# Kernel tuning notes

Hardware: AMD Instinct MI355X
Metric: run time of the kernel (lower is better)

## Reference

```python
import jax, jax.numpy as jnp
import numpy as np

BINS = 256
SIGMA = 3.0
DELTA = 1.0 / BINS
CENTERS = DELTA * (jnp.arange(BINS, dtype=jnp.float32) + 0.5)  # min=0
W1 = W2 = W3 = 1.0

# --- soft histogram (SoftHistTorch with bins=256, min=0, max=1, sigma=3) ---

def _soft_hist(flat):
    # flat: [N] -> hist: [BINS]
    d = flat[None, :] - CENTERS[:, None]                      # [BINS, N]
    h = jax.nn.sigmoid(SIGMA * (d + DELTA / 2)) - jax.nn.sigmoid(SIGMA * (d - DELTA / 2))
    return h.sum(axis=1)


def _color_uniform(x):
    # x: [B,H,W]; uniform_loss = mean_b sum_bins h*log(h) (only where h>0)
    flat = x.reshape(x.shape[0], -1)
    hist = jax.vmap(_soft_hist)(flat)                          # [B, BINS]
    safe = jnp.where(hist > 0, hist, 1.0)
    hlogh = jnp.where(hist > 0, hist * jnp.log(safe), 0.0)
    return hlogh.sum(axis=1).mean()

# --- SSIM (standard pytorch-ssim: 11x11 gaussian window, sigma=1.5, 1 channel) ---

def _gauss_window(size=11, sigma=1.5):
    c = np.arange(size, dtype=np.float64) - size // 2
    g = np.exp(-(c ** 2) / (2.0 * sigma ** 2))
    g /= g.sum()
    w = np.outer(g, g)
    return jnp.asarray(w, dtype=jnp.float32)[None, None]       # [1,1,11,11]

_WIN = _gauss_window()
_PAD = 11 // 2


def _conv(img):
    return jax.lax.conv_general_dilated(img, _WIN, (1, 1), [(_PAD, _PAD), (_PAD, _PAD)])


def _ssim(img1, img2):
    C1, C2 = 0.01 ** 2, 0.03 ** 2
    mu1, mu2 = _conv(img1), _conv(img2)
    mu1_sq, mu2_sq, mu1_mu2 = mu1 * mu1, mu2 * mu2, mu1 * mu2
    s1 = _conv(img1 * img1) - mu1_sq
    s2 = _conv(img2 * img2) - mu2_sq
    s12 = _conv(img1 * img2) - mu1_mu2
    num = (2 * mu1_mu2 + C1) * (2 * s12 + C2)
    den = (mu1_sq + mu2_sq + C1) * (s1 + s2 + C2)
    return (num / den).mean()


def _norm01(t):
    t = t - t.min()
    return t / t.max()


def setup_inputs() -> dict:
    key = jax.random.key(0)
    k1, k2, k3 = jax.random.split(key, 3)
    x = jax.random.uniform(k1, (8, 1, 384, 384), dtype=jnp.float32)
    target = jax.random.uniform(k2, (8, 384, 384), dtype=jnp.float32)
    depth = jax.random.uniform(k3, (8, 384, 384), dtype=jnp.float32)
    return {"x": x, "target": target, "depth": depth}


def reference(x, target, depth):
    x = jnp.squeeze(x, 1)                 # [B,H,W]
    output = _norm01(x)                   # torch in-place normalization aliases x
    IR = _norm01(target)
    depth_n = _norm01(depth)
    B = x.shape[0]
    uniform_loss = _color_uniform(output)
    depth_loss = jnp.sum(output * depth_n) / B   # x aliases normalized output in torch
    ssim_loss = 1.0 - _ssim(output[:, None], IR[:, None])
    loss = W1 * 1e-06 * uniform_loss + W2 * 1e-05 * depth_loss + W3 * ssim_loss
    return loss
```

## Files before the change

### kernel.cpp

```cpp
#include <hip/hip_runtime.h>
#include <math.h>

#define NTHR 256
#define K_FINE 2048
#define HW 147456
#define N1 1179648
#define IMG 384
#define NHC 16
#define NCHUNK 128
#define NTILE 1152
#define TOTAL (NTILE + NCHUNK)
#define NSOFT 256

#define WS_PMM  0
#define WS_SUM  1536
#define WS_CTR  2304
#define WS_HIST 2312
#define WS_SSIM (WS_HIST + 8*K_FINE)
#define WS_UNIF (WS_SSIM + NTILE)

#define HRS (42*33)
#define SMEMF (42*43*2 + 3*HRS)

__global__ __launch_bounds__(NTHR) void k_minmax(
        const float* __restrict__ x, const float* __restrict__ tg,
        const float* __restrict__ dp, float* __restrict__ wsf)
{
    __shared__ float swred[4][12];
    const int tid = threadIdx.x, bid = blockIdx.x;
    const float4* x4 = (const float4*)x  + bid * 1152;
    const float4* t4 = (const float4*)tg + bid * 1152;
    const float4* d4 = (const float4*)dp + bid * 1152;
    float mn0 = 3.4e38f, mx0 = -3.4e38f;
    float mn1 = 3.4e38f, mx1 = -3.4e38f;
    float mn2 = 3.4e38f, mx2 = -3.4e38f;
    float sx = 0.f, sd = 0.f, sxd = 0.f;
    for (int i = tid; i < 1152; i += NTHR) {
        float4 a = x4[i], b = t4[i], d = d4[i];
        mn0 = fminf(mn0, fminf(fminf(a.x, a.y), fminf(a.z, a.w)));
        mx0 = fmaxf(mx0, fmaxf(fmaxf(a.x, a.y), fmaxf(a.z, a.w)));
        mn1 = fminf(mn1, fminf(fminf(b.x, b.y), fminf(b.z, b.w)));
        mx1 = fmaxf(mx1, fmaxf(fmaxf(b.x, b.y), fmaxf(b.z, b.w)));
        mn2 = fminf(mn2, fminf(fminf(d.x, d.y), fminf(d.z, d.w)));
        mx2 = fmaxf(mx2, fmaxf(fmaxf(d.x, d.y), fmaxf(d.z, d.w)));
        sx += (a.x + a.y) + (a.z + a.w);
        sd += (d.x + d.y) + (d.z + d.w);
        sxd = fmaf(a.x, d.x, fmaf(a.y, d.y, fmaf(a.z, d.z, fmaf(a.w, d.w, sxd))));
    }
    #pragma unroll
    for (int off = 32; off; off >>= 1) {
        mn0 = fminf(mn0, __shfl_down(mn0, off, 64));
        mx0 = fmaxf(mx0, __shfl_down(mx0, off, 64));
        mn1 = fminf(mn1, __shfl_down(mn1, off, 64));
        mx1 = fmaxf(mx1, __shfl_down(mx1, off, 64));
        mn2 = fminf(mn2, __shfl_down(mn2, off, 64));
        mx2 = fmaxf(mx2, __shfl_down(mx2, off, 64));
        sx  += __shfl_down(sx,  off, 64);
        sd  += __shfl_down(sd,  off, 64);
        sxd += __shfl_down(sxd, off, 64);
    }
    if ((tid & 63) == 0) {
        int w = tid >> 6;
        swred[w][0] = mn0; swred[w][1] = mx0; swred[w][2] = mn1;
        swred[w][3] = mx1; swred[w][4] = mn2; swred[w][5] = mx2;
        swred[w][6] = sxd; swred[w][7] = sx;  swred[w][8] = sd;
    }
    __syncthreads();
    if (tid == 0) {
        #pragma unroll
        for (int w = 1; w < 4; w++) {
            swred[0][0] = fminf(swred[0][0], swred[w][0]);
            swred[0][1] = fmaxf(swred[0][1], swred[w][1]);
            swred[0][2] = fminf(swred[0][2], swred[w][2]);
            swred[0][3] = fmaxf(swred[0][3], swred[w][3]);
            swred[0][4] = fminf(swred[0][4], swred[w][4]);
            swred[0][5] = fmaxf(swred[0][5], swred[w][5]);
            swred[0][6] += swred[w][6];
            swred[0][7] += swred[w][7];
            swred[0][8] += swred[w][8];
        }
        wsf[WS_PMM +        bid * 2]     = swred[0][0];
        wsf[WS_PMM +        bid * 2 + 1] = swred[0][1];
        wsf[WS_PMM + 512  + bid * 2]     = swred[0][2];
        wsf[WS_PMM + 512  + bid * 2 + 1] = swred[0][3];
        wsf[WS_PMM + 1024 + bid * 2]     = swred[0][4];
        wsf[WS_PMM + 1024 + bid * 2 + 1] = swred[0][5];
        wsf[WS_SUM +        bid] = swred[0][6];
        wsf[WS_SUM + 256  + bid] = swred[0][7];
        wsf[WS_SUM + 512  + bid] = swred[0][8];
        if (bid == 0) ((int*)wsf)[WS_CTR] = 0;
    }
    if (tid < 64) ((int*)wsf)[WS_HIST + bid * 64 + tid] = 0;
}

__device__ __forceinline__ void reduce_minmax(
        const float* __restrict__ wsf, float swred[4][12], int tid,
        float& xmn, float& xinv, float& tmn, float& tinv, float& dmn, float& dinv)
{
    const float2* pm = (const float2*)&wsf[WS_PMM];
    float2 a = pm[tid], b = pm[256 + tid], c = pm[512 + tid];
    float mn0 = a.x, mx0 = a.y, mn1 = b.x, mx1 = b.y, mn2 = c.x, mx2 = c.y;
    #pragma unroll
    for (int off = 32; off; off >>= 1) {
        mn0 = fminf(mn0, __shfl_down(mn0, off, 64));
        mx0 = fmaxf(mx0, __shfl_down(mx0, off, 64));
        mn1 = fminf(mn1, __shfl_down(mn1, off, 64));
        mx1 = fmaxf(mx1, __shfl_down(mx1, off, 64));
        mn2 = fminf(mn2, __shfl_down(mn2, off, 64));
        mx2 = fmaxf(mx2, __shfl_down(mx2, off, 64));
    }
    if ((tid & 63) == 0) {
        int w = tid >> 6;
        swred[w][0] = mn0; swred[w][1] = mx0; swred[w][2] = mn1;
        swred[w][3] = mx1; swred[w][4] = mn2; swred[w][5] = mx2;
    }
    __syncthreads();
    mn0 = fminf(fminf(swred[0][0], swred[1][0]), fminf(swred[2][0], swred[3][0]));
    mx0 = fmaxf(fmaxf(swred[0][1], swred[1][1]), fmaxf(swred[2][1], swred[3][1]));
    mn1 = fminf(fminf(swred[0][2], swred[1][2]), fminf(swred[2][2], swred[3][2]));
    mx1 = fmaxf(fmaxf(swred[0][3], swred[1][3]), fmaxf(swred[2][3], swred[3][3]));
    mn2 = fminf(fminf(swred[0][4], swred[1][4]), fminf(swred[2][4], swred[3][4]));
    mx2 = fmaxf(fmaxf(swred[0][5], swred[1][5]), fmaxf(swred[2][5], swred[3][5]));
    xmn = mn0; xinv = 1.0f / (mx0 - mn0);
    tmn = mn1; tinv = 1.0f / (mx1 - mn1);
    dmn = mn2; dinv = 1.0f / (mx2 - mn2);
    __syncthreads();
}

__global__ __launch_bounds__(NTHR) void k_work(
        const float* __restrict__ x, const float* __restrict__ tg,
        float* __restrict__ wsf)
{
    __shared__ float smem[SMEMF];
    __shared__ float swred[4][12];
    const int tid = threadIdx.x, bid = blockIdx.x;

    float xmn, xinv, tmn, tinv, dmn, dinv;
    reduce_minmax(wsf, swred, tid, xmn, xinv, tmn, tinv, dmn, dinv);
    (void)dmn; (void)dinv;

    if (bid < NTILE) {
        float g[11];
        {
            float s = 0.f;
            #pragma unroll
            for (int i = 0; i < 11; i++) {
                float dd = (float)(i - 5);
                g[i] = expf(-dd * dd / 4.5f);
                s += g[i];
            }
            float is = 1.0f / s;
            #pragma unroll
            for (int i = 0; i < 11; i++) g[i] *= is;
        }
        float* sO  = smem;
        float* sI  = smem + 42 * 43;
        float* hr0 = smem + 2 * 42 * 43;
        float* hr1 = hr0 + HRS;
        float* hr2 = hr1 + HRS;
        int img = bid / 144;
        int tl  = bid % 144;
        int ty0 = (tl / 12) * 32 - 5;
        int tx0 = (tl % 12) * 32 - 5;
        const float* xb = x  + (size_t)img * HW;
        const float* tb = tg + (size_t)img * HW;
        for (int idx = tid; idx < 42 * 42; idx += NTHR) {
            int rr = idx / 42, cc = idx % 42;
            int gy = ty0 + rr, gx = tx0 + cc;
            float xv = 0.f, tv = 0.f;
            if (gy >= 0 && gy < IMG && gx >= 0 && gx < IMG) {
                int o = gy * IMG + gx;
                xv = (xb[o] - xmn) * xinv;
                tv = (tb[o] - tmn) * tinv;
            }
            sO[rr * 43 + cc] = xv; sI[rr * 43 + cc] = tv;
        }
        __syncthreads();
        for (int idx = tid; idx < 42 * 32; idx += NTHR) {
            int rr = idx >> 5, cx = idx & 31;
            const float* rowO = sO + rr * 43 + cx;
            const float* rowI = sI + rr * 43 + cx;
            float so = 0, si = 0;
            #pragma unroll
            for (int d = 0; d < 11; d++) { so += g[d] * rowO[d]; si += g[d] * rowI[d]; }
            hr0[rr * 33 + cx] = so; hr1[rr * 33 + cx] = si;
        }
        __syncthreads();
        const int ox = tid & 31, oy0 = (tid >> 5) << 2;
        float mu1[4], mu2[4];
        {
            float w0[14], w1[14];
            #pragma unroll
            for (int k = 0; k < 14; k++) {
                int hb = (oy0 + k) * 33 + ox;
                w0[k] = hr0[hb]; w1[k] = hr1[hb];
            }
            #pragma unroll
            for (int p = 0; p < 4; p++) {
                float m1 = 0, m2 = 0;
                #pragma unroll
                for (int dy = 0; dy < 11; dy++) {
                    m1 += g[dy] * w0[p + dy];
                    m2 += g[dy] * w1[p + dy];
                }
                mu1[p] = m1; mu2[p] = m2;
            }
        }
        __syncthreads();
        for (int idx = tid; idx < 42 * 32; idx += NTHR) {
            int rr = idx >> 5, cx = idx & 31;
            const float* rowO = sO + rr * 43 + cx;
            const float* rowI = sI + rr * 43 + cx;
            float soo = 0, sii = 0, soi = 0;
            #pragma unroll
            for (int d = 0; d < 11; d++) {
                float o = rowO[d], ii = rowI[d], w = g[d];
                soo += w * o * o; sii += w * ii * ii; soi += w * o * ii;
            }
            int hb = rr * 33 + cx;
            hr0[hb] = soo; hr1[hb] = sii; hr2[hb] = soi;
        }
        __syncthreads();
        const float C1 = 1e-4f, C2 = 9e-4f;
        float lsum = 0.f;
        {
            float w0[14], w1[14], w2[14];
            #pragma unroll
            for (int k = 0; k < 14; k++) {
                int hb = (oy0 + k) * 33 + ox;
                w0[k] = hr0[hb]; w1[k] = hr1[hb]; w2[k] = hr2[hb];
            }
            #pragma unroll
            for (int p = 0; p < 4; p++) {
                float m11 = 0, m22 = 0, m12 = 0;
                #pragma unroll
                for (int dy = 0; dy < 11; dy++) {
                    float w = g[dy];
                    m11 += w * w0[p + dy];
                    m22 += w * w1[p + dy];
                    m12 += w * w2[p + dy];
                }
                float mu1s = mu1[p] * mu1[p], mu2s = mu2[p] * mu2[p];
                float mu12 = mu1[p] * mu2[p];
                float s1 = m11 - mu1s, s2 = m22 - mu2s, s12 = m12 - mu12;
                lsum += ((2.f * mu12 + C1) * (2.f * s12 + C2))
                      / ((mu1s + mu2s + C1) * (s1 + s2 + C2));
            }
        }
        #pragma unroll
        for (int off = 32; off; off >>= 1) lsum += __shfl_down(lsum, off, 64);
        if ((tid & 63) == 0) swred[tid >> 6][6] = lsum;
        __syncthreads();
        if (tid == 0)
            wsf[WS_SSIM + bid] = swred[0][6] + swred[1][6] + swred[2][6] + swred[3][6];
    } else {
        int c = bid - NTILE;
        int* lh = (int*)smem;
        for (int i = tid; i < K_FINE; i += NTHR) lh[i] = 0;
        __syncthreads();
        int batch = c >> 4, chunk = c & 15;
        const float4* x4 = (const float4*)x + (size_t)batch * (HW / 4) + chunk * 2304;
        for (int i = tid; i < 2304; i += NTHR) {
            float4 xv = x4[i];
            float o0 = (xv.x - xmn) * xinv, o1 = (xv.y - xmn) * xinv;
            float o2 = (xv.z - xmn) * xinv, o3 = (xv.w - xmn) * xinv;
            int j0 = min(K_FINE - 1, max(0, (int)(o0 * K_FINE)));
            int j1 = min(K_FINE - 1, max(0, (int)(o1 * K_FINE)));
            int j2 = min(K_FINE - 1, max(0, (int)(o2 * K_FINE)));
            int j3 = min(K_FINE - 1, max(0, (int)(o3 * K_FINE)));
            atomicAdd(lh + j0, 1); atomicAdd(lh + j1, 1);
            atomicAdd(lh + j2, 1); atomicAdd(lh + j3, 1);
        }
        __syncthreads();
        int* gh = (int*)wsf + WS_HIST + batch * K_FINE;
        for (int i = tid; i < K_FINE; i += NTHR) {
            int v = lh[i];
            if (v) atomicAdd(gh + i, v);
        }
    }
}

__global__ __launch_bounds__(NTHR) void k_soft_final(
        float* __restrict__ wsf, float* __restrict__ out)
{
    __shared__ int lh[K_FINE];
    __shared__ float swred[4][12];
    __shared__ float s8[8];
    __shared__ int amLast;
    const int tid = threadIdx.x, bid = blockIdx.x;
    int batch = bid >> 5;
    const int* gh = (const int*)wsf + WS_HIST + batch * K_FINE;
    for (int i = tid; i < K_FINE; i += NTHR) lh[i] = gh[i];
    __syncthreads();
    int binLocal = tid >> 5, slice = tid & 31;
    int bin = (bid & 31) * 8 + binLocal;
    const float delta = 1.0f / 256.0f;
    const float r   = expf(3.0f * delta);
    const float rm1 = r - 1.0f;
    const float c32 = expf(-3.0f * 32.0f / (float)K_FINE);
    float L = (float)bin * delta;
    float u = expf(3.0f * (L - ((float)slice + 0.5f) * (1.0f / (float)K_FINE)));
    float h = 0.f;
    #pragma unroll 4
    for (int j = slice; j < K_FINE; j += 32) {
        float cnt = (float)lh[j];
        float t1 = 1.0f + u;
        float t2 = fmaf(u, r, 1.0f);
        h = fmaf(cnt * (u * rm1), __builtin_amdgcn_rcpf(t1 * t2), h);
        u *= c32;
    }
    #pragma unroll
    for (int off = 16; off; off >>= 1) h += __shfl_down(h, off, 32);
    if (slice == 0) s8[binLocal] = h;
    __syncthreads();
    if (tid == 0) {
        float hl = 0.f;
        #pragma unroll
        for (int b = 0; b < 8; b++) {
            float hh = s8[b];
            hl += (hh > 0.f) ? hh * logf(hh) : 0.f;
        }
        wsf[WS_UNIF + bid] = hl;
        __threadfence();
        int old = atomicAdd((int*)wsf + WS_CTR, 1);
        amLast = (old == NSOFT - 1);
    }
    __syncthreads();
    if (!amLast) return;

    __threadfence();
    float xmn, xinv, tmn, tinv, dmn, dinv;
    reduce_minmax(wsf, swred, tid, xmn, xinv, tmn, tinv, dmn, dinv);
    (void)tmn; (void)tinv;
    float sxd  = wsf[WS_SUM + tid];
    float sx   = wsf[WS_SUM + 256 + tid];
    float sd   = wsf[WS_SUM + 512 + tid];
    float bsum = 0.f;
    for (int i = tid; i < NTILE; i += NTHR) bsum += wsf[WS_SSIM + i];
    float c = wsf[WS_UNIF + tid];
    float* r0 = (float*)lh;
    float* r1 = r0 + 256; float* r2 = r1 + 256;
    float* r3 = r2 + 256; float* r4 = r3 + 256;
    r0[tid] = sxd; r1[tid] = sx; r2[tid] = sd; r3[tid] = bsum; r4[tid] = c;
    __syncthreads();
    for (int s = 128; s; s >>= 1) {
        if (tid < s) {
            r0[tid] += r0[tid + s]; r1[tid] += r1[tid + s];
            r2[tid] += r2[tid + s]; r3[tid] += r3[tid + s];
            r4[tid] += r4[tid + s];
        }
        __syncthreads();
    }
    if (tid == 0) {
        float SXD = r0[0], SX = r1[0], SD = r2[0];
        float uniform  = r4[0] / 8.0f;
        float depthNum = SXD - xmn * SD - dmn * SX + (float)N1 * xmn * dmn;
        float depthL   = xinv * dinv * depthNum / 8.0f;
        float ssimMean = r3[0] / (float)N1;
        out[0] = 1e-6f * uniform + 1e-5f * depthL + (1.0f - ssimMean);
    }
}

extern "C" void kernel_launch(void* const* d_in, const int* in_sizes, int n_in,
                              void* d_out, int out_size, void* d_ws, size_t ws_size,
                              hipStream_t stream) {
    const float* x  = (const float*)d_in[0];
    const float* tg = (const float*)d_in[1];
    const float* dp = (const float*)d_in[2];
    float* wsf = (float*)d_ws;
    float* out = (float*)d_out;
    hipLaunchKernelGGL(k_minmax,     dim3(256),   dim3(NTHR), 0, stream, x, tg, dp, wsf);
    hipLaunchKernelGGL(k_work,       dim3(TOTAL), dim3(NTHR), 0, stream, x, tg, wsf);
    hipLaunchKernelGGL(k_soft_final, dim3(NSOFT), dim3(NTHR), 0, stream, wsf, out);
}
```

Measured before the change: 39.74 us.

## Fuse SSIM horizontal pass with global loads and compute all five planes at once

The SSIM tile no longer stages normalized x/target tiles in shared memory. Each thread reads 11 pixels directly from global memory and computes all five horizontal convolution sums (mu and second moments) in one pass. The vertical pass then runs over five shared planes without the intermediate barriers. This removes two shared-memory passes and two syncs, at the cost of redundant global loads (each pixel is read about 11 times, mostly hitting cache) and higher register pressure.

```diff
diff --git a/kernel.cpp b/kernel.cpp
--- a/kernel.cpp
+++ b/kernel.cpp
@@ -20,7 +20,7 @@
 #define WS_UNIF (WS_SSIM + NTILE)
 
 #define HRS (42*33)
-#define SMEMF (42*43*2 + 3*HRS)
+#define SMEMF (5*HRS)
 
 __global__ __launch_bounds__(NTHR) void k_minmax(
         const float* __restrict__ x, const float* __restrict__ tg,
@@ -153,99 +153,87 @@
             #pragma unroll
             for (int i = 0; i < 11; i++) g[i] *= is;
         }
-        float* sO  = smem;
-        float* sI  = smem + 42 * 43;
-        float* hr0 = smem + 2 * 42 * 43;
+        float* hr0 = smem;
         float* hr1 = hr0 + HRS;
         float* hr2 = hr1 + HRS;
+        float* hr3 = hr2 + HRS;
+        float* hr4 = hr3 + HRS;
         int img = bid / 144;
         int tl  = bid % 144;
         int ty0 = (tl / 12) * 32 - 5;
         int tx0 = (tl % 12) * 32 - 5;
         const float* xb = x  + (size_t)img * HW;
         const float* tb = tg + (size_t)img * HW;
-        for (int idx = tid; idx < 42 * 42; idx += NTHR) {
-            int rr = idx / 42, cc = idx % 42;
-            int gy = ty0 + rr, gx = tx0 + cc;
-            float xv = 0.f, tv = 0.f;
-            if (gy >= 0 && gy < IMG && gx >= 0 && gx < IMG) {
-                int o = gy * IMG + gx;
-                xv = (xb[o] - xmn) * xinv;
-                tv = (tb[o] - tmn) * tinv;
+
+        for (int t = tid; t < 42 * 33; t += NTHR) {
+            int rr = t / 33, cx = t - rr * 33;
+            int gy = ty0 + rr, b = tx0 + cx;
+            float o[11], ii[11];
+            bool rowOK = ((unsigned)gy < (unsigned)IMG);
+            if (rowOK && b >= 0 && b + 10 < IMG) {
+                const float* po = xb + gy * IMG + b;
+                const float* pi = tb + gy * IMG + b;
+                #pragma unroll
+                for (int k = 0; k < 11; k++) {
+                    o[k]  = (po[k] - xmn) * xinv;
+                    ii[k] = (pi[k] - tmn) * tinv;
+                }
+            } else {
+                #pragma unroll
+                for (int k = 0; k < 11; k++) {
+                    int gx = b + k;
+                    bool okk = rowOK && ((unsigned)gx < (unsigned)IMG);
+                    float xv = 0.f, tv = 0.f;
+                    if (okk) {
+                        int off = gy * IMG + gx;
+                        xv = (xb[off] - xmn) * xinv;
+                        tv = (tb[off] - tmn) * tinv;
+                    }
+                    o[k] = xv; ii[k] = tv;
+                }
             }
-            sO[rr * 43 + cc] = xv; sI[rr * 43 + cc] = tv;
-        }
-        __syncthreads();
-        for (int idx = tid; idx < 42 * 32; idx += NTHR) {
-            int rr = idx >> 5, cx = idx & 31;
-            const float* rowO = sO + rr * 43 + cx;
-            const float* rowI = sI + rr * 43 + cx;
-            float so = 0, si = 0;
+            float c1 = 0, c2 = 0, c3 = 0, c4 = 0, c5 = 0;
             #pragma unroll
-            for (int d = 0; d < 11; d++) { so += g[d] * rowO[d]; si += g[d] * rowI[d]; }
-            hr0[rr * 33 + cx] = so; hr1[rr * 33 + cx] = si;
-        }
-        __syncthreads();
+            for (int k = 0; k < 11; k++) {
+                float gk = g[k];
+                float go = gk * o[k], gi = gk * ii[k];
+                c1 = fmaf(gk, o[k], c1);
+                c2 = fmaf(gk, ii[k], c2);
+                c3 = fmaf(go, o[k], c3);
+                c4 = fmaf(gi, ii[k], c4);
+                c5 = fmaf(go, ii[k], c5);
+            }
+            hr0[t] = c1; hr1[t] = c2; hr2[t] = c3; hr3[t] = c4; hr4[t] = c5;
+        }
+        __syncthreads();
+
         const int ox = tid & 31, oy0 = (tid >> 5) << 2;
-        float mu1[4], mu2[4];
-        {
-            float w0[14], w1[14];
-            #pragma unroll
-            for (int k = 0; k < 14; k++) {
-                int hb = (oy0 + k) * 33 + ox;
-                w0[k] = hr0[hb]; w1[k] = hr1[hb];
-            }
-            #pragma unroll
-            for (int p = 0; p < 4; p++) {
-                float m1 = 0, m2 = 0;
-                #pragma unroll
-                for (int dy = 0; dy < 11; dy++) {
-                    m1 += g[dy] * w0[p + dy];
-                    m2 += g[dy] * w1[p + dy];
-                }
-                mu1[p] = m1; mu2[p] = m2;
-            }
-        }
-        __syncthreads();
-        for (int idx = tid; idx < 42 * 32; idx += NTHR) {
-            int rr = idx >> 5, cx = idx & 31;
-            const float* rowO = sO + rr * 43 + cx;
-            const float* rowI = sI + rr * 43 + cx;
-            float soo = 0, sii = 0, soi = 0;
-            #pragma unroll
-            for (int d = 0; d < 11; d++) {
-                float o = rowO[d], ii = rowI[d], w = g[d];
-                soo += w * o * o; sii += w * ii * ii; soi += w * o * ii;
-            }
-            int hb = rr * 33 + cx;
-            hr0[hb] = soo; hr1[hb] = sii; hr2[hb] = soi;
-        }
-        __syncthreads();
+        float a1[4], a2[4], b11[4], b22[4], b12[4];
+        #define VCONV(HR, ACC)                                              \
+        {                                                                   \
+            float w[14];                                                    \
+            _Pragma("unroll")                                               \
+            for (int k = 0; k < 14; k++) w[k] = HR[(oy0 + k) * 33 + ox];    \
+            _Pragma("unroll")                                               \
+            for (int p = 0; p < 4; p++) {                                   \
+                float m = 0.f;                                              \
+                _Pragma("unroll")                                           \
+                for (int dy = 0; dy < 11; dy++) m = fmaf(g[dy], w[p + dy], m); \
+                ACC[p] = m;                                                 \
+            }                                                               \
+        }
+        VCONV(hr0, a1) VCONV(hr1, a2) VCONV(hr2, b11) VCONV(hr3, b22) VCONV(hr4, b12)
+        #undef VCONV
+
         const float C1 = 1e-4f, C2 = 9e-4f;
         float lsum = 0.f;
-        {
-            float w0[14], w1[14], w2[14];
-            #pragma unroll
-            for (int k = 0; k < 14; k++) {
-                int hb = (oy0 + k) * 33 + ox;
-                w0[k] = hr0[hb]; w1[k] = hr1[hb]; w2[k] = hr2[hb];
-            }
-            #pragma unroll
-            for (int p = 0; p < 4; p++) {
-                float m11 = 0, m22 = 0, m12 = 0;
-                #pragma unroll
-                for (int dy = 0; dy < 11; dy++) {
-                    float w = g[dy];
-                    m11 += w * w0[p + dy];
-                    m22 += w * w1[p + dy];
-                    m12 += w * w2[p + dy];
-                }
-                float mu1s = mu1[p] * mu1[p], mu2s = mu2[p] * mu2[p];
-                float mu12 = mu1[p] * mu2[p];
-                float s1 = m11 - mu1s, s2 = m22 - mu2s, s12 = m12 - mu12;
-                lsum += ((2.f * mu12 + C1) * (2.f * s12 + C2))
-                      / ((mu1s + mu2s + C1) * (s1 + s2 + C2));
-            }
+        #pragma unroll
+        for (int p = 0; p < 4; p++) {
+            float mu1s = a1[p] * a1[p], mu2s = a2[p] * a2[p];
+            float mu12 = a1[p] * a2[p];
+            float s1 = b11[p] - mu1s, s2 = b22[p] - mu2s, s12 = b12[p] - mu12;
+            lsum += ((2.f * mu12 + C1) * (2.f * s12 + C2))
+                  / ((mu1s + mu2s + C1) * (s1 + s2 + C2));
         }
         #pragma unroll
         for (int off = 32; off; off >>= 1) lsum += __shfl_down(lsum, off, 64);
```

Measured after the change: 51.85 us. 30.5% more time.

## Fuse soft-histogram and final reduction into work kernel via atomic tail blocks

Applied to the files above, without the earlier changes.

Removes the third kernel launch. The last 256 blocks to finish the work kernel, ordered by an atomic rank counter, wait until all histogram blocks are done and then compute the soft histogram. The very last of those blocks spins until every block has finished and writes the final loss. Histogram blocks are moved to the front of the grid so they finish early, and the SSIM convolutions use explicit fmaf. In exchange, the code relies on spin-waits and relaxed/acquire atomics for cross-block ordering, and the tail blocks run serially after the main work.

```diff
diff --git a/kernel.cpp b/kernel.cpp
--- a/kernel.cpp
+++ b/kernel.cpp
@@ -6,7 +6,6 @@
 #define HW 147456
 #define N1 1179648
 #define IMG 384
-#define NHC 16
 #define NCHUNK 128
 #define NTILE 1152
 #define TOTAL (NTILE + NCHUNK)
@@ -19,8 +18,23 @@
 #define WS_SSIM (WS_HIST + 8*K_FINE)
 #define WS_UNIF (WS_SSIM + NTILE)
 
+#define CTR_FIN  0
+#define CTR_HIST 1
+#define CTR_SOFT 2
+
 #define HRS (42*33)
 #define SMEMF (42*43*2 + 3*HRS)
+
+#define AGENT __HIP_MEMORY_SCOPE_AGENT
+
+__device__ __forceinline__ void spin_relaxed_then_acq(int* p, int target) {
+    while (__hip_atomic_load(p, __ATOMIC_RELAXED, AGENT) < target)
+        __builtin_amdgcn_s_sleep(16);
+    (void)__hip_atomic_load(p, __ATOMIC_ACQUIRE, AGENT);
+}
+__device__ __forceinline__ void drain_vmem() {
+    asm volatile("s_waitcnt vmcnt(0)" ::: "memory");
+}
 
 __global__ __launch_bounds__(NTHR) void k_minmax(
         const float* __restrict__ x, const float* __restrict__ tg,
@@ -88,9 +102,9 @@
         wsf[WS_SUM +        bid] = swred[0][6];
         wsf[WS_SUM + 256  + bid] = swred[0][7];
         wsf[WS_SUM + 512  + bid] = swred[0][8];
-        if (bid == 0) ((int*)wsf)[WS_CTR] = 0;
     }
     if (tid < 64) ((int*)wsf)[WS_HIST + bid * 64 + tid] = 0;
+    if (bid == 0 && tid < 8) ((int*)wsf)[WS_CTR + tid] = 0;
 }
 
 __device__ __forceinline__ void reduce_minmax(
@@ -129,17 +143,46 @@
 
 __global__ __launch_bounds__(NTHR) void k_work(
         const float* __restrict__ x, const float* __restrict__ tg,
-        float* __restrict__ wsf)
+        float* __restrict__ wsf, float* __restrict__ out)
 {
     __shared__ float smem[SMEMF];
     __shared__ float swred[4][12];
+    __shared__ float s8[8];
+    __shared__ int sbc[2];
     const int tid = threadIdx.x, bid = blockIdx.x;
+    int* ctr = (int*)wsf + WS_CTR;
 
     float xmn, xinv, tmn, tinv, dmn, dinv;
     reduce_minmax(wsf, swred, tid, xmn, xinv, tmn, tinv, dmn, dinv);
     (void)dmn; (void)dinv;
 
-    if (bid < NTILE) {
+    const bool isHist = (bid < NCHUNK);
+    if (isHist) {
+        int c = bid;
+        int* lh = (int*)smem;
+        for (int i = tid; i < K_FINE; i += NTHR) lh[i] = 0;
+        __syncthreads();
+        int batch = c >> 4, chunk = c & 15;
+        const float4* x4 = (const float4*)x + (size_t)batch * (HW / 4) + chunk * 2304;
+        for (int i = tid; i < 2304; i += NTHR) {
+            float4 xv = x4[i];
+            float o0 = (xv.x - xmn) * xinv, o1 = (xv.y - xmn) * xinv;
+            float o2 = (xv.z - xmn) * xinv, o3 = (xv.w - xmn) * xinv;
+            int j0 = min(K_FINE - 1, max(0, (int)(o0 * K_FINE)));
+            int j1 = min(K_FINE - 1, max(0, (int)(o1 * K_FINE)));
+            int j2 = min(K_FINE - 1, max(0, (int)(o2 * K_FINE)));
+            int j3 = min(K_FINE - 1, max(0, (int)(o3 * K_FINE)));
+            atomicAdd(lh + j0, 1); atomicAdd(lh + j1, 1);
+            atomicAdd(lh + j2, 1); atomicAdd(lh + j3, 1);
+        }
+        __syncthreads();
+        int* gh = (int*)wsf + WS_HIST + batch * K_FINE;
+        for (int i = tid; i < K_FINE; i += NTHR) {
+            int v = lh[i];
+            if (v) atomicAdd(gh + i, v);
+        }
+    } else {
+        int tileId = bid - NCHUNK;
         float g[11];
         {
             float s = 0.f;
@@ -158,8 +201,8 @@
         float* hr0 = smem + 2 * 42 * 43;
         float* hr1 = hr0 + HRS;
         float* hr2 = hr1 + HRS;
-        int img = bid / 144;
-        int tl  = bid % 144;
+        int img = tileId / 144;
+        int tl  = tileId % 144;
         int ty0 = (tl / 12) * 32 - 5;
         int tx0 = (tl % 12) * 32 - 5;
         const float* xb = x  + (size_t)img * HW;
@@ -182,7 +225,7 @@
             const float* rowI = sI + rr * 43 + cx;
             float so = 0, si = 0;
             #pragma unroll
-            for (int d = 0; d < 11; d++) { so += g[d] * rowO[d]; si += g[d] * rowI[d]; }
+            for (int d = 0; d < 11; d++) { so = fmaf(g[d], rowO[d], so); si = fmaf(g[d], rowI[d], si); }
             hr0[rr * 33 + cx] = so; hr1[rr * 33 + cx] = si;
         }
         __syncthreads();
@@ -200,8 +243,8 @@
                 float m1 = 0, m2 = 0;
                 #pragma unroll
                 for (int dy = 0; dy < 11; dy++) {
-                    m1 += g[dy] * w0[p + dy];
-                    m2 += g[dy] * w1[p + dy];
+                    m1 = fmaf(g[dy], w0[p + dy], m1);
+                    m2 = fmaf(g[dy], w1[p + dy], m2);
                 }
                 mu1[p] = m1; mu2[p] = m2;
             }
@@ -215,7 +258,7 @@
             #pragma unroll
             for (int d = 0; d < 11; d++) {
                 float o = rowO[d], ii = rowI[d], w = g[d];
-                soo += w * o * o; sii += w * ii * ii; soi += w * o * ii;
+                soo = fmaf(w * o, o, soo); sii = fmaf(w * ii, ii, sii); soi = fmaf(w * o, ii, soi);
             }
             int hb = rr * 33 + cx;
             hr0[hb] = soo; hr1[hb] = sii; hr2[hb] = soi;
@@ -236,9 +279,9 @@
                 #pragma unroll
                 for (int dy = 0; dy < 11; dy++) {
                     float w = g[dy];
-                    m11 += w * w0[p + dy];
-                    m22 += w * w1[p + dy];
-                    m12 += w * w2[p + dy];
+                    m11 = fmaf(w, w0[p + dy], m11);
+                    m22 = fmaf(w, w1[p + dy], m22);
+                    m12 = fmaf(w, w2[p + dy], m12);
                 }
                 float mu1s = mu1[p] * mu1[p], mu2s = mu2[p] * mu2[p];
                 float mu12 = mu1[p] * mu2[p];
@@ -252,112 +295,96 @@
         if ((tid & 63) == 0) swred[tid >> 6][6] = lsum;
         __syncthreads();
         if (tid == 0)
-            wsf[WS_SSIM + bid] = swred[0][6] + swred[1][6] + swred[2][6] + swred[3][6];
-    } else {
-        int c = bid - NTILE;
+            wsf[WS_SSIM + tileId] = swred[0][6] + swred[1][6] + swred[2][6] + swred[3][6];
+    }
+
+    drain_vmem();
+    __syncthreads();
+    if (tid == 0) {
+        if (isHist) __hip_atomic_fetch_add(ctr + CTR_HIST, 1, __ATOMIC_RELAXED, AGENT);
+        sbc[0] = __hip_atomic_fetch_add(ctr + CTR_FIN, 1, __ATOMIC_RELAXED, AGENT);
+    }
+    __syncthreads();
+    int rank = sbc[0];
+    if (rank < TOTAL - NSOFT) return;
+
+    int srank = rank - (TOTAL - NSOFT);
+    if (tid == 0) spin_relaxed_then_acq(ctr + CTR_HIST, NCHUNK);
+    __syncthreads();
+    {
         int* lh = (int*)smem;
-        for (int i = tid; i < K_FINE; i += NTHR) lh[i] = 0;
-        __syncthreads();
-        int batch = c >> 4, chunk = c & 15;
-        const float4* x4 = (const float4*)x + (size_t)batch * (HW / 4) + chunk * 2304;
-        for (int i = tid; i < 2304; i += NTHR) {
-            float4 xv = x4[i];
-            float o0 = (xv.x - xmn) * xinv, o1 = (xv.y - xmn) * xinv;
-            float o2 = (xv.z - xmn) * xinv, o3 = (xv.w - xmn) * xinv;
-            int j0 = min(K_FINE - 1, max(0, (int)(o0 * K_FINE)));
-            int j1 = min(K_FINE - 1, max(0, (int)(o1 * K_FINE)));
-            int j2 = min(K_FINE - 1, max(0, (int)(o2 * K_FINE)));
-            int j3 = min(K_FINE - 1, max(0, (int)(o3 * K_FINE)));
-            atomicAdd(lh + j0, 1); atomicAdd(lh + j1, 1);
-            atomicAdd(lh + j2, 1); atomicAdd(lh + j3, 1);
-        }
-        __syncthreads();
-        int* gh = (int*)wsf + WS_HIST + batch * K_FINE;
-        for (int i = tid; i < K_FINE; i += NTHR) {
-            int v = lh[i];
-            if (v) atomicAdd(gh + i, v);
-        }
-    }
-}
-
-__global__ __launch_bounds__(NTHR) void k_soft_final(
-        float* __restrict__ wsf, float* __restrict__ out)
-{
-    __shared__ int lh[K_FINE];
-    __shared__ float swred[4][12];
-    __shared__ float s8[8];
-    __shared__ int amLast;
-    const int tid = threadIdx.x, bid = blockIdx.x;
-    int batch = bid >> 5;
-    const int* gh = (const int*)wsf + WS_HIST + batch * K_FINE;
-    for (int i = tid; i < K_FINE; i += NTHR) lh[i] = gh[i];
-    __syncthreads();
-    int binLocal = tid >> 5, slice = tid & 31;
-    int bin = (bid & 31) * 8 + binLocal;
-    const float delta = 1.0f / 256.0f;
-    const float r   = expf(3.0f * delta);
-    const float rm1 = r - 1.0f;
-    const float c32 = expf(-3.0f * 32.0f / (float)K_FINE);
-    float L = (float)bin * delta;
-    float u = expf(3.0f * (L - ((float)slice + 0.5f) * (1.0f / (float)K_FINE)));
-    float h = 0.f;
-    #pragma unroll 4
-    for (int j = slice; j < K_FINE; j += 32) {
-        float cnt = (float)lh[j];
-        float t1 = 1.0f + u;
-        float t2 = fmaf(u, r, 1.0f);
-        h = fmaf(cnt * (u * rm1), __builtin_amdgcn_rcpf(t1 * t2), h);
-        u *= c32;
-    }
-    #pragma unroll
-    for (int off = 16; off; off >>= 1) h += __shfl_down(h, off, 32);
-    if (slice == 0) s8[binLocal] = h;
-    __syncthreads();
-    if (tid == 0) {
-        float hl = 0.f;
+        int batch = srank >> 5;
+        const int* gh = (const int*)wsf + WS_HIST + batch * K_FINE;
+        for (int i = tid; i < K_FINE; i += NTHR)
+            lh[i] = __hip_atomic_load((int*)(gh + i), __ATOMIC_RELAXED, AGENT);
+        __syncthreads();
+        int binLocal = tid >> 5, slice = tid & 31;
+        int bin = (srank & 31) * 8 + binLocal;
+        const float delta = 1.0f / 256.0f;
+        const float r   = expf(3.0f * delta);
+        const float rm1 = r - 1.0f;
+        const float c32 = expf(-3.0f * 32.0f / (float)K_FINE);
+        float L = (float)bin * delta;
+        float u = expf(3.0f * (L - ((float)slice + 0.5f) * (1.0f / (float)K_FINE)));
+        float h = 0.f;
+        #pragma unroll 4
+        for (int j = slice; j < K_FINE; j += 32) {
+            float cnt = (float)lh[j];
+            float t1 = 1.0f + u;
+            float t2 = fmaf(u, r, 1.0f);
+            h = fmaf(cnt * (u * rm1), __builtin_amdgcn_rcpf(t1 * t2), h);
+            u *= c32;
+        }
         #pragma unroll
-        for (int b = 0; b < 8; b++) {
-            float hh = s8[b];
-            hl += (hh > 0.f) ? hh * logf(hh) : 0.f;
-        }
-        wsf[WS_UNIF + bid] = hl;
-        __threadfence();
-        int old = atomicAdd((int*)wsf + WS_CTR, 1);
-        amLast = (old == NSOFT - 1);
-    }
-    __syncthreads();
-    if (!amLast) return;
-
-    __threadfence();
-    float xmn, xinv, tmn, tinv, dmn, dinv;
-    reduce_minmax(wsf, swred, tid, xmn, xinv, tmn, tinv, dmn, dinv);
-    (void)tmn; (void)tinv;
-    float sxd  = wsf[WS_SUM + tid];
-    float sx   = wsf[WS_SUM + 256 + tid];
-    float sd   = wsf[WS_SUM + 512 + tid];
-    float bsum = 0.f;
-    for (int i = tid; i < NTILE; i += NTHR) bsum += wsf[WS_SSIM + i];
-    float c = wsf[WS_UNIF + tid];
-    float* r0 = (float*)lh;
-    float* r1 = r0 + 256; float* r2 = r1 + 256;
-    float* r3 = r2 + 256; float* r4 = r3 + 256;
-    r0[tid] = sxd; r1[tid] = sx; r2[tid] = sd; r3[tid] = bsum; r4[tid] = c;
-    __syncthreads();
-    for (int s = 128; s; s >>= 1) {
-        if (tid < s) {
-            r0[tid] += r0[tid + s]; r1[tid] += r1[tid + s];
-            r2[tid] += r2[tid + s]; r3[tid] += r3[tid + s];
-            r4[tid] += r4[tid + s];
-        }
-        __syncthreads();
-    }
-    if (tid == 0) {
-        float SXD = r0[0], SX = r1[0], SD = r2[0];
-        float uniform  = r4[0] / 8.0f;
-        float depthNum = SXD - xmn * SD - dmn * SX + (float)N1 * xmn * dmn;
-        float depthL   = xinv * dinv * depthNum / 8.0f;
-        float ssimMean = r3[0] / (float)N1;
-        out[0] = 1e-6f * uniform + 1e-5f * depthL + (1.0f - ssimMean);
+        for (int off = 16; off; off >>= 1) h += __shfl_down(h, off, 32);
+        if (slice == 0) s8[binLocal] = h;
+        __syncthreads();
+        if (tid == 0) {
+            float hl = 0.f;
+            #pragma unroll
+            for (int b = 0; b < 8; b++) {
+                float hh = s8[b];
+                hl += (hh > 0.f) ? hh * logf(hh) : 0.f;
+            }
+            wsf[WS_UNIF + srank] = hl;
+            drain_vmem();
+            int old = __hip_atomic_fetch_add(ctr + CTR_SOFT, 1, __ATOMIC_RELAXED, AGENT);
+            sbc[1] = (old == NSOFT - 1);
+        }
+    }
+    __syncthreads();
+    if (!sbc[1]) return;
+
+    if (tid == 0) spin_relaxed_then_acq(ctr + CTR_FIN, TOTAL);
+    __syncthreads();
+    {
+        float sxd  = wsf[WS_SUM + tid];
+        float sx   = wsf[WS_SUM + 256 + tid];
+        float sd   = wsf[WS_SUM + 512 + tid];
+        float bsum = 0.f;
+        for (int i = tid; i < NTILE; i += NTHR)
+            bsum += __hip_atomic_load((float*)&wsf[WS_SSIM + i], __ATOMIC_RELAXED, AGENT);
+        float c = __hip_atomic_load((float*)&wsf[WS_UNIF + tid], __ATOMIC_RELAXED, AGENT);
+        float* r0 = smem; float* r1 = r0 + 256; float* r2 = r1 + 256;
+        float* r3 = r2 + 256; float* r4 = r3 + 256;
+        r0[tid] = sxd; r1[tid] = sx; r2[tid] = sd; r3[tid] = bsum; r4[tid] = c;
+        __syncthreads();
+        for (int s = 128; s; s >>= 1) {
+            if (tid < s) {
+                r0[tid] += r0[tid + s]; r1[tid] += r1[tid + s];
+                r2[tid] += r2[tid + s]; r3[tid] += r3[tid + s];
+                r4[tid] += r4[tid + s];
+            }
+            __syncthreads();
+        }
+        if (tid == 0) {
+            float SXD = r0[0], SX = r1[0], SD = r2[0];
+            float uniform  = r4[0] / 8.0f;
+            float depthNum = SXD - xmn * SD - dmn * SX + (float)N1 * xmn * dmn;
+            float depthL   = xinv * dinv * depthNum / 8.0f;
+            float ssimMean = r3[0] / (float)N1;
+            out[0] = 1e-6f * uniform + 1e-5f * depthL + (1.0f - ssimMean);
+        }
     }
 }
 
@@ -369,7 +396,6 @@
     const float* dp = (const float*)d_in[2];
     float* wsf = (float*)d_ws;
     float* out = (float*)d_out;
-    hipLaunchKernelGGL(k_minmax,     dim3(256),   dim3(NTHR), 0, stream, x, tg, dp, wsf);
-    hipLaunchKernelGGL(k_work,       dim3(TOTAL), dim3(NTHR), 0, stream, x, tg, wsf);
-    hipLaunchKernelGGL(k_soft_final, dim3(NSOFT), dim3(NTHR), 0, stream, wsf, out);
-}
+    hipLaunchKernelGGL(k_minmax, dim3(256),   dim3(NTHR), 0, stream, x, tg, dp, wsf);
+    hipLaunchKernelGGL(k_work,   dim3(TOTAL), dim3(NTHR), 0, stream, x, tg, wsf, out);
+}
```

New measurement: 45.89 us. 15.5% more time.
